# Optimization experiments

Hardware: AMD Instinct MI355X
Metric: run time of the kernel (lower is better)

Reference implementation:

```python
import jax, jax.numpy as jnp
import numpy as np

NEG_SLOPE = 0.2  # PyG GATConv default LeakyReLU slope


def _leaky_relu(x):
    return jnp.where(x >= 0, x, NEG_SLOPE * x)


def gat_conv(x, edge_index, W, a_src, a_dst, b, concat):
    """Faithful PyG GATConv: gather -> leakyrelu attention -> per-dst softmax -> scatter.
    x: [N, Fin], edge_index: [2, E] (src, dst), W: [Fin, H*C], a_src/a_dst: [H, C], b: [H*C] or [C].
    """
    N = x.shape[0]
    H, C = a_src.shape
    src, dst = edge_index[0], edge_index[1]
    h = (x @ W).reshape(N, H, C)                       # [N, H, C]
    alpha_s = jnp.einsum('nhc,hc->nh', h, a_src)       # [N, H]
    alpha_d = jnp.einsum('nhc,hc->nh', h, a_dst)       # [N, H]
    e = _leaky_relu(alpha_s[src] + alpha_d[dst])       # [E, H]
    # numerically stable softmax over edges grouped by destination node
    m = jax.ops.segment_max(e, dst, num_segments=N)    # [N, H]
    e = jnp.exp(e - m[dst])                            # [E, H]
    denom = jax.ops.segment_sum(e, dst, num_segments=N)  # [N, H]
    alpha = e / denom[dst]                             # [E, H]
    msg = h[src] * alpha[:, :, None]                   # [E, H, C]
    out = jax.ops.segment_sum(msg, dst, num_segments=N)  # [N, H, C]
    out = out.reshape(N, H * C) if concat else out.mean(axis=1)
    return out + b


def setup_inputs() -> dict:
    key = jax.random.key(0)
    ks = jax.random.split(key, 12)
    N, E, Fin, Fout = 100000, 1600000, 256, 40
    H1, C1 = 8, 8
    x = jax.random.normal(ks[0], (N, Fin), dtype=jnp.float32)
    edge_index = jax.random.randint(ks[1], (2, E), 0, N, dtype=jnp.int64)
    g = lambda k, shape: jax.random.normal(k, shape, dtype=jnp.float32) * np.float32(np.sqrt(2.0 / (shape[0] + shape[-1])))
    return {
        'x': x,
        'edge_index': edge_index,
        'W1': g(ks[2], (Fin, H1 * C1)),
        'a1_src': g(ks[3], (H1, C1)),
        'a1_dst': g(ks[4], (H1, C1)),
        'b1': jnp.zeros((H1 * C1,), dtype=jnp.float32),
        'W2': g(ks[5], (H1 * C1, Fout)),
        'a2_src': g(ks[6], (1, Fout)),
        'a2_dst': g(ks[7], (1, Fout)),
        'b2': jnp.zeros((Fout,), dtype=jnp.float32),
    }


def reference(x, edge_index, W1, a1_src, a1_dst, b1, W2, a2_src, a2_dst, b2):
    N = x.shape[0]
    # PyG GATConv adds self-loops by default
    loops = jnp.arange(N, dtype=edge_index.dtype)
    ei = jnp.concatenate([edge_index, jnp.stack([loops, loops])], axis=1)
    h = gat_conv(x, ei, W1, a1_src, a1_dst, b1, concat=True)   # [N, 64]
    h = jax.nn.relu(h)  # F.dropout is identity in eval mode
    h = gat_conv(h, ei, W2, a2_src, a2_dst, b2, concat=False)  # [N, Fout]
    return jax.nn.log_softmax(h, axis=1)
```

## Files before the change

### kernel.cpp

```cpp
#include <hip/hip_runtime.h>
#include <math.h>

#define NEG_SLOPE 0.2f
__device__ __forceinline__ float lrelu(float x){ return x >= 0.f ? x : NEG_SLOPE * x; }

typedef __attribute__((ext_vector_type(8))) short bf16x8;
typedef __attribute__((ext_vector_type(4))) float f32x4;

__device__ __forceinline__ float wred_sum(float v){
  #pragma unroll
  for (int o = 32; o; o >>= 1) v += __shfl_xor(v, o, 64);
  return v;
}

__device__ __forceinline__ float bfhi_f(float f){
  return __uint_as_float(__float_as_uint(f) & 0xFFFF0000u);
}
__device__ __forceinline__ unsigned short f2bf(float f){
  unsigned u = __float_as_uint(f);
  unsigned r = u + 0x7FFFu + ((u >> 16) & 1u);
  return (unsigned short)(r >> 16);
}

__global__ __launch_bounds__(256) void k_prep(const int* __restrict__ ei, int E, int N, int nb, int cb,
    unsigned* __restrict__ bcnt,
    const float* __restrict__ W1, short* __restrict__ wt_hi, short* __restrict__ wt_lo,
    const float* __restrict__ W2, short* __restrict__ wt2_hi, short* __restrict__ wt2_lo){
  __shared__ unsigned h[512];
  int bid = blockIdx.x;
  if (bid < cb){
    const int tot = E + N;
    for (int i = threadIdx.x; i < nb; i += 256) h[i] = 0;
    __syncthreads();
    int base = bid * 8192;
    #pragma unroll 4
    for (int j = 0; j < 32; j++){
      int e = base + threadIdx.x + j * 256;
      if (e < tot){
        unsigned d = (e < E) ? (unsigned)ei[E + e] : (unsigned)(e - E);
        atomicAdd(&h[d >> 8], 1u);
      }
    }
    __syncthreads();
    for (int i = threadIdx.x; i < nb; i += 256)
      if (h[i]) atomicAdd(&bcnt[i], h[i]);
  } else if (bid < cb + 64){
    int i = (bid - cb) * 256 + threadIdx.x;
    int k = i >> 6, c = i & 63;
    float v = W1[i];
    unsigned u = __float_as_uint(v);
    wt_hi[c * 256 + k] = (short)(u >> 16);
    float lo = v - bfhi_f(v);
    wt_lo[c * 256 + k] = (short)(__float_as_uint(lo) >> 16);
  } else {
    int i = (bid - cb - 64) * 256 + threadIdx.x;
    if (i < 48 * 64){
      int c = i >> 6, k = i & 63;
      float v = (c < 40) ? W2[k * 40 + c] : 0.f;
      unsigned u = __float_as_uint(v);
      wt2_hi[c * 64 + k] = (short)(u >> 16);
      float l = v - bfhi_f(v);
      wt2_lo[c * 64 + k] = (short)(__float_as_uint(l) >> 16);
    }
  }
}

__global__ void k_bscan(const unsigned* __restrict__ bcnt, unsigned* __restrict__ bbase,
                        unsigned* __restrict__ bcur, int nb, int tot){
  __shared__ unsigned s[512];
  int t = threadIdx.x;
  unsigned v = (t < nb) ? bcnt[t] : 0u;
  s[t] = v; __syncthreads();
  for (int off = 1; off < 512; off <<= 1){
    unsigned x = (t >= off) ? s[t - off] : 0u; __syncthreads();
    s[t] += x; __syncthreads();
  }
  if (t < nb){ unsigned b = s[t] - v; bbase[t] = b; bcur[t] = b; }
  if (t == 0) bbase[nb] = (unsigned)tot;
}

__global__ __launch_bounds__(256) void k_binscat(const int* __restrict__ ei, int E, int N, int nb,
    unsigned* __restrict__ bcur, unsigned* __restrict__ staged){
  __shared__ unsigned sd[8192];
  __shared__ unsigned hist[512];
  __shared__ unsigned runb[512];
  const int tot = E + N;
  for (int i = threadIdx.x; i < nb; i += 256) hist[i] = 0;
  __syncthreads();
  int base = blockIdx.x * 8192;
  #pragma unroll 4
  for (int j = 0; j < 32; j++){
    int idx = threadIdx.x + j * 256;
    int e = base + idx;
    unsigned d = 0xFFFFFFFFu;
    if (e < tot) d = (e < E) ? (unsigned)ei[E + e] : (unsigned)(e - E);
    sd[idx] = d;
    if (d != 0xFFFFFFFFu) atomicAdd(&hist[d >> 8], 1u);
  }
  __syncthreads();
  for (int i = threadIdx.x; i < nb; i += 256){
    unsigned c = hist[i];
    runb[i] = c ? atomicAdd(&bcur[i], c) : 0u;
    hist[i] = 0;
  }
  __syncthreads();
  #pragma unroll 4
  for (int j = 0; j < 32; j++){
    int idx = threadIdx.x + j * 256;
    unsigned d = sd[idx];
    if (d == 0xFFFFFFFFu) continue;
    int e = base + idx;
    unsigned s = (e < E) ? (unsigned)ei[e] : d;
    unsigned b = d >> 8;
    unsigned pos = runb[b] + atomicAdd(&hist[b], 1u);
    staged[pos] = s | ((d & 255u) << 20);
  }
}

__global__ __launch_bounds__(256) void k_csrgemm1(
    const unsigned* __restrict__ bbase, const unsigned* __restrict__ staged, int nb,
    unsigned* __restrict__ off_, unsigned* __restrict__ cur, int* __restrict__ srcids,
    const float* __restrict__ x,
    const unsigned* __restrict__ wtu_hi, const unsigned* __restrict__ wtu_lo,
    const float* __restrict__ a1s, const float* __restrict__ a1d,
    unsigned short* __restrict__ h1b, float* __restrict__ as_, float* __restrict__ ad_, int N){
  __shared__ union {
    struct { unsigned cnt[256], scn[256], cnt2[256]; } c;
    unsigned B[2][64 * 132];
  } sm;

  if (blockIdx.x < nb){
    int b = blockIdx.x, t = threadIdx.x;
    unsigned beg = bbase[b], end = bbase[b + 1];
    sm.c.cnt[t] = 0; sm.c.cnt2[t] = 0;
    __syncthreads();
    for (unsigned i = beg + t; i < end; i += 256)
      atomicAdd(&sm.c.cnt[staged[i] >> 20], 1u);
    __syncthreads();
    unsigned v = sm.c.cnt[t];
    sm.c.scn[t] = v; __syncthreads();
    for (int off = 1; off < 256; off <<= 1){
      unsigned xval = (t >= off) ? sm.c.scn[t - off] : 0u; __syncthreads();
      sm.c.scn[t] += xval; __syncthreads();
    }
    unsigned ex = sm.c.scn[t] - v;
    int d = b * 256 + t;
    if (d < N){ off_[d] = beg + ex; cur[d] = beg + ex + v; }
    sm.c.cnt[t] = ex;
    __syncthreads();
    for (unsigned i = beg + t; i < end; i += 256){
      unsigned u = staged[i];
      unsigned dl = u >> 20;
      unsigned pos = beg + sm.c.cnt[dl] + atomicAdd(&sm.c.cnt2[dl], 1u);
      srcids[pos] = (int)(u & 0xFFFFFu);
    }
    return;
  }

  int bid  = blockIdx.x - nb;
  int lane = threadIdx.x & 63;
  int wv   = threadIdx.x >> 6;
  int r0   = bid * 64 + wv * 16;
  int col16 = lane & 15;
  int kg    = lane >> 4;

  #pragma unroll
  for (int j = 0; j < 32; j++){
    int g = threadIdx.x + j * 256;
    int row = g >> 7, col = g & 127;
    sm.B[0][row * 132 + col] = wtu_hi[g];
    sm.B[1][row * 132 + col] = wtu_lo[g];
  }
  __syncthreads();
  if (r0 >= N) return;

  const float* xr = x + (size_t)min(r0 + col16, N - 1) * 256 + kg * 8;

  f32x4 acc[4];
  #pragma unroll
  for (int ct = 0; ct < 4; ct++) acc[ct] = (f32x4){0.f, 0.f, 0.f, 0.f};

  #pragma unroll 2
  for (int kt = 0; kt < 8; kt++){
    float4 v0 = *(const float4*)(xr + kt * 32);
    float4 v1 = *(const float4*)(xr + kt * 32 + 4);
    unsigned u[8] = {__float_as_uint(v0.x), __float_as_uint(v0.y), __float_as_uint(v0.z), __float_as_uint(v0.w),
                     __float_as_uint(v1.x), __float_as_uint(v1.y), __float_as_uint(v1.z), __float_as_uint(v1.w)};
    union { bf16x8 v; unsigned u[4]; } ahi, alo;
    #pragma unroll
    for (int j = 0; j < 4; j++)
      ahi.u[j] = __builtin_amdgcn_perm(u[2*j+1], u[2*j], 0x07060302);
    float lo[8];
    lo[0] = v0.x - bfhi_f(v0.x); lo[1] = v0.y - bfhi_f(v0.y);
    lo[2] = v0.z - bfhi_f(v0.z); lo[3] = v0.w - bfhi_f(v0.w);
    lo[4] = v1.x - bfhi_f(v1.x); lo[5] = v1.y - bfhi_f(v1.y);
    lo[6] = v1.z - bfhi_f(v1.z); lo[7] = v1.w - bfhi_f(v1.w);
    #pragma unroll
    for (int j = 0; j < 4; j++)
      alo.u[j] = __builtin_amdgcn_perm(__float_as_uint(lo[2*j+1]), __float_as_uint(lo[2*j]), 0x07060302);

    #pragma unroll
    for (int ct = 0; ct < 4; ct++){
      int wcol = ct * 16 + col16;
      const bf16x8 bhi = *(const bf16x8*)(&sm.B[0][wcol * 132 + kt * 16 + kg * 4]);
      const bf16x8 blo = *(const bf16x8*)(&sm.B[1][wcol * 132 + kt * 16 + kg * 4]);
      acc[ct] = __builtin_amdgcn_mfma_f32_16x16x32_bf16(ahi.v, bhi, acc[ct], 0, 0, 0);
      acc[ct] = __builtin_amdgcn_mfma_f32_16x16x32_bf16(ahi.v, blo, acc[ct], 0, 0, 0);
      acc[ct] = __builtin_amdgcn_mfma_f32_16x16x32_bf16(alo.v, bhi, acc[ct], 0, 0, 0);
    }
  }

  float cs[4], cd[4];
  #pragma unroll
  for (int ct = 0; ct < 4; ct++){ cs[ct] = a1s[ct * 16 + col16]; cd[ct] = a1d[ct * 16 + col16]; }
  #pragma unroll
  for (int r = 0; r < 4; r++){
    int rr = r0 + kg * 4 + r;
    bool ok = rr < N;
    #pragma unroll
    for (int ct = 0; ct < 4; ct++){
      float v = acc[ct][r];
      if (ok) h1b[(size_t)rr * 64 + ct * 16 + col16] = f2bf(v);
      float s = v * cs[ct];
      float t = v * cd[ct];
      s += __shfl_xor(s, 1, 64); s += __shfl_xor(s, 2, 64); s += __shfl_xor(s, 4, 64);
      t += __shfl_xor(t, 1, 64); t += __shfl_xor(t, 2, 64); t += __shfl_xor(t, 4, 64);
      if (ok && (col16 & 7) == 0){
        int head = ct * 2 + (col16 >> 3);
        as_[(size_t)rr * 8 + head] = s;
        ad_[(size_t)rr * 8 + head] = t;
      }
    }
  }
}

__global__ __launch_bounds__(256) void k_gat1(const unsigned* __restrict__ off_, const unsigned* __restrict__ cur,
    const int* __restrict__ srcids, const float* __restrict__ as_, const float* __restrict__ ad_,
    const unsigned short* __restrict__ h1b, const float* __restrict__ b1,
    unsigned short* __restrict__ out1b, int N){
  int lane = threadIdx.x & 63;
  int wv   = threadIdx.x >> 6;
  int d    = blockIdx.x * 4 + wv;
  if (d >= N) return;
  __shared__ float lds_p[4][64 * 8];
  __shared__ int   lds_s[4][64];
  float* lp = lds_p[wv];
  int*   ls = lds_s[wv];
  unsigned beg = off_[d], fin = cur[d];

  int e8 = lane >> 3, h = lane & 7;
  int c0 = lane & 31, pe = lane >> 5, hh = c0 >> 2;
  float adh = ad_[(size_t)d * 8 + h];
  float psacc = 0.f, accx = 0.f, accy = 0.f;

  for (unsigned base = beg; base < fin; base += 64){
    int nthis = (int)min(64u, fin - base);
    unsigned i = base + lane;
    ls[lane] = (i < fin) ? srcids[i] : 0;
    asm volatile("s_waitcnt lgkmcnt(0)" ::: "memory");
    __builtin_amdgcn_sched_barrier(0);
    for (int j = 0; j < nthis; j += 8){
      int eloc = j + e8;
      int s = ls[eloc];
      float p = 0.f;
      if (eloc < nthis) p = __expf(lrelu(as_[(size_t)s * 8 + h] + adh));
      lp[eloc * 8 + h] = p;
      psacc += p;
    }
    asm volatile("s_waitcnt lgkmcnt(0)" ::: "memory");
    __builtin_amdgcn_sched_barrier(0);
    for (int e = 0; e < nthis; e += 8){
      int e0 = e + pe, e1 = e + 2 + pe, e2 = e + 4 + pe, e3 = e + 6 + pe;
      float p0 = lp[e0 * 8 + hh], p1 = lp[e1 * 8 + hh];
      float p2 = lp[e2 * 8 + hh], p3 = lp[e3 * 8 + hh];
      int s0 = ls[e0], s1 = ls[e1], s2 = ls[e2], s3 = ls[e3];
      unsigned u0 = *(const unsigned*)(h1b + (size_t)s0 * 64 + c0 * 2);
      unsigned u1 = *(const unsigned*)(h1b + (size_t)s1 * 64 + c0 * 2);
      unsigned u2 = *(const unsigned*)(h1b + (size_t)s2 * 64 + c0 * 2);
      unsigned u3 = *(const unsigned*)(h1b + (size_t)s3 * 64 + c0 * 2);
      accx = fmaf(p0, __uint_as_float(u0 << 16), accx);
      accy = fmaf(p0, __uint_as_float(u0 & 0xFFFF0000u), accy);
      accx = fmaf(p1, __uint_as_float(u1 << 16), accx);
      accy = fmaf(p1, __uint_as_float(u1 & 0xFFFF0000u), accy);
      accx = fmaf(p2, __uint_as_float(u2 << 16), accx);
      accy = fmaf(p2, __uint_as_float(u2 & 0xFFFF0000u), accy);
      accx = fmaf(p3, __uint_as_float(u3 << 16), accx);
      accy = fmaf(p3, __uint_as_float(u3 & 0xFFFF0000u), accy);
    }
    asm volatile("" ::: "memory");
  }
  float den = psacc;
  den += __shfl_xor(den, 8, 64);
  den += __shfl_xor(den, 16, 64);
  den += __shfl_xor(den, 32, 64);
  float mydenv = __shfl(den, hh, 64);
  accx += __shfl_xor(accx, 32, 64);
  accy += __shfl_xor(accy, 32, 64);
  if (lane < 32){
    int ch = lane * 2;
    float v0 = accx / mydenv + b1[ch];
    float v1 = accy / mydenv + b1[ch + 1];
    ushort2 o;
    o.x = f2bf(v0 > 0.f ? v0 : 0.f);
    o.y = f2bf(v1 > 0.f ? v1 : 0.f);
    *(ushort2*)(out1b + (size_t)d * 64 + ch) = o;
  }
}

__global__ __launch_bounds__(256) void k_gemm2m(const unsigned short* __restrict__ out1b,
    const short* __restrict__ wt2_hi, const short* __restrict__ wt2_lo,
    const float* __restrict__ a2s, const float* __restrict__ a2d,
    unsigned short* __restrict__ h2b, float* __restrict__ as_, float* __restrict__ ad_, int N){
  int lane = threadIdx.x & 63;
  int wv   = threadIdx.x >> 6;
  int r0   = blockIdx.x * 64 + wv * 16;
  if (r0 >= N) return;
  int col16 = lane & 15;
  int kg    = lane >> 4;
  const unsigned short* ar = out1b + (size_t)min(r0 + col16, N - 1) * 64 + kg * 8;

  f32x4 acc[3];
  #pragma unroll
  for (int ct = 0; ct < 3; ct++) acc[ct] = (f32x4){0.f, 0.f, 0.f, 0.f};

  #pragma unroll
  for (int kt = 0; kt < 2; kt++){
    const bf16x8 a = *(const bf16x8*)(ar + kt * 32);
    #pragma unroll
    for (int ct = 0; ct < 3; ct++){
      int wcol = ct * 16 + col16;
      const bf16x8 bhi = *(const bf16x8*)(wt2_hi + wcol * 64 + kt * 32 + kg * 8);
      const bf16x8 blo = *(const bf16x8*)(wt2_lo + wcol * 64 + kt * 32 + kg * 8);
      acc[ct] = __builtin_amdgcn_mfma_f32_16x16x32_bf16(a, bhi, acc[ct], 0, 0, 0);
      acc[ct] = __builtin_amdgcn_mfma_f32_16x16x32_bf16(a, blo, acc[ct], 0, 0, 0);
    }
  }

  float cs[3], cd[3];
  #pragma unroll
  for (int ct = 0; ct < 3; ct++){
    int col = ct * 16 + col16;
    bool okc = col < 40;
    cs[ct] = okc ? a2s[col] : 0.f;
    cd[ct] = okc ? a2d[col] : 0.f;
  }
  #pragma unroll
  for (int r = 0; r < 4; r++){
    int rr = r0 + kg * 4 + r;
    bool ok = rr < N;
    float s = 0.f, t = 0.f;
    #pragma unroll
    for (int ct = 0; ct < 3; ct++){
      s = fmaf(acc[ct][r], cs[ct], s);
      t = fmaf(acc[ct][r], cd[ct], t);
      int col = ct * 16 + col16;
      if (ok && col < 40) h2b[(size_t)rr * 40 + col] = f2bf(acc[ct][r]);
    }
    s += __shfl_xor(s, 1, 64); s += __shfl_xor(s, 2, 64);
    s += __shfl_xor(s, 4, 64); s += __shfl_xor(s, 8, 64);
    t += __shfl_xor(t, 1, 64); t += __shfl_xor(t, 2, 64);
    t += __shfl_xor(t, 4, 64); t += __shfl_xor(t, 8, 64);
    if (ok && col16 == 0){ as_[rr] = s; ad_[rr] = t; }
  }
}

__global__ __launch_bounds__(256) void k_gat2(const unsigned* __restrict__ off_, const unsigned* __restrict__ cur,
    const int* __restrict__ srcids, const float* __restrict__ as_, const float* __restrict__ ad_,
    const unsigned short* __restrict__ h2b, const float* __restrict__ b2, float* __restrict__ out, int N){
  int lane = threadIdx.x & 63;
  int wv   = threadIdx.x >> 6;
  int d    = blockIdx.x * 4 + wv;
  if (d >= N) return;
  __shared__ float lds_p[4][64];
  __shared__ int   lds_s[4][64];
  float* lp = lds_p[wv];
  int*   ls = lds_s[wv];
  unsigned beg = off_[d], fin = cur[d];
  float add = ad_[d];

  int c0 = lane & 31;
  int pe = lane >> 5;
  int idx = c0 < 20 ? c0 : 19;
  float ps = 0.f, accx = 0.f, accy = 0.f;

  for (unsigned base = beg; base < fin; base += 64){
    unsigned i = base + lane;
    int nthis = (int)min(64u, fin - base);
    if (i < fin){
      int s = srcids[i];
      float p = __expf(lrelu(as_[s] + add));
      ps += p; ls[lane] = s; lp[lane] = p;
    } else { ls[lane] = 0; lp[lane] = 0.f; }
    asm volatile("s_waitcnt lgkmcnt(0)" ::: "memory");
    __builtin_amdgcn_sched_barrier(0);
    for (int e = 0; e < nthis; e += 8){
      int e0 = e + pe, e1 = e + 2 + pe, e2 = e + 4 + pe, e3 = e + 6 + pe;
      float p0 = lp[e0], p1 = lp[e1], p2 = lp[e2], p3 = lp[e3];
      int s0 = ls[e0], s1 = ls[e1], s2 = ls[e2], s3 = ls[e3];
      unsigned u0 = *(const unsigned*)(h2b + (size_t)s0 * 40 + idx * 2);
      unsigned u1 = *(const unsigned*)(h2b + (size_t)s1 * 40 + idx * 2);
      unsigned u2 = *(const unsigned*)(h2b + (size_t)s2 * 40 + idx * 2);
      unsigned u3 = *(const unsigned*)(h2b + (size_t)s3 * 40 + idx * 2);
      accx = fmaf(p0, __uint_as_float(u0 << 16), accx);
      accy = fmaf(p0, __uint_as_float(u0 & 0xFFFF0000u), accy);
      accx = fmaf(p1, __uint_as_float(u1 << 16), accx);
      accy = fmaf(p1, __uint_as_float(u1 & 0xFFFF0000u), accy);
      accx = fmaf(p2, __uint_as_float(u2 << 16), accx);
      accy = fmaf(p2, __uint_as_float(u2 & 0xFFFF0000u), accy);
      accx = fmaf(p3, __uint_as_float(u3 << 16), accx);
      accy = fmaf(p3, __uint_as_float(u3 & 0xFFFF0000u), accy);
    }
    asm volatile("" ::: "memory");
  }
  ps = wred_sum(ps);
  accx += __shfl_xor(accx, 32, 64);
  accy += __shfl_xor(accy, 32, 64);

  float v0 = accx / ps + b2[idx * 2];
  float v1 = accy / ps + b2[idx * 2 + 1];
  bool act = (c0 < 20);
  float mx = act ? fmaxf(v0, v1) : -INFINITY;
  #pragma unroll
  for (int o = 16; o; o >>= 1) mx = fmaxf(mx, __shfl_xor(mx, o, 64));
  float exs = act ? (__expf(v0 - mx) + __expf(v1 - mx)) : 0.f;
  #pragma unroll
  for (int o = 16; o; o >>= 1) exs += __shfl_xor(exs, o, 64);
  float lse = mx + logf(exs);
  if (lane < 20){
    float2 o2; o2.x = v0 - lse; o2.y = v1 - lse;
    *(float2*)(out + (size_t)d * 40 + lane * 2) = o2;
  }
}

extern "C" void kernel_launch(void* const* d_in, const int* in_sizes, int n_in,
                              void* d_out, int out_size, void* d_ws, size_t ws_size,
                              hipStream_t stream){
  const float* x   = (const float*)d_in[0];
  const int*   ei  = (const int*)d_in[1];
  const float* W1  = (const float*)d_in[2];
  const float* a1s = (const float*)d_in[3];
  const float* a1d = (const float*)d_in[4];
  const float* b1  = (const float*)d_in[5];
  const float* W2  = (const float*)d_in[6];
  const float* a2s = (const float*)d_in[7];
  const float* a2d = (const float*)d_in[8];
  const float* b2  = (const float*)d_in[9];
  float* out = (float*)d_out;

  const int N = in_sizes[0] / 256;
  const int E = in_sizes[1] / 2;
  const int tot = E + N;
  const int nb  = (N + 255) >> 8;

  float* ws = (float*)d_ws;
  size_t o = 0;
  float* as1  = ws + o; o += (size_t)N * 8;
  float* ad1  = ws + o; o += (size_t)N * 8;
  unsigned short* out1b = (unsigned short*)(ws + o); o += (size_t)N * 32;
  unsigned short* h1b   = (unsigned short*)(ws + o); o += (size_t)N * 32;
  unsigned short* h2b   = (unsigned short*)(ws + o); o += (size_t)N * 20;
  unsigned* off_ = (unsigned*)(ws + o); o += (size_t)N;
  unsigned* cur  = (unsigned*)(ws + o); o += (size_t)N;
  int* srcids    = (int*)(ws + o);      o += (size_t)tot;
  short* wt_hi   = (short*)(ws + o);    o += 8192;
  short* wt_lo   = (short*)(ws + o);    o += 8192;
  short* wt2_hi  = (short*)(ws + o);    o += 1536;
  short* wt2_lo  = (short*)(ws + o);    o += 1536;
  unsigned* bcnt  = (unsigned*)(ws + o); o += nb;
  unsigned* bbase = (unsigned*)(ws + o); o += nb + 1;
  unsigned* bcur  = (unsigned*)(ws + o); o += nb;
  unsigned* staged = (unsigned*)out1b;
  float* as2 = as1;
  float* ad2 = ad1;

  const int cb = (tot + 8191) / 8192;
  const int gb = (N + 63) / 64;

  hipMemsetAsync(bcnt, 0, sizeof(unsigned) * (size_t)nb, stream);

  k_prep   <<<cb + 64 + 12, 256, 0, stream>>>(ei, E, N, nb, cb, bcnt,
                                              W1, wt_hi, wt_lo, W2, wt2_hi, wt2_lo);
  k_bscan  <<<1, 512, 0, stream>>>(bcnt, bbase, bcur, nb, tot);
  k_binscat<<<cb, 256, 0, stream>>>(ei, E, N, nb, bcur, staged);

  k_csrgemm1<<<nb + gb, 256, 0, stream>>>(bbase, staged, nb, off_, cur, srcids,
                                          x, (const unsigned*)wt_hi, (const unsigned*)wt_lo,
                                          a1s, a1d, h1b, as1, ad1, N);
  k_gat1 <<<(N + 3) / 4, 256, 0, stream>>>(off_, cur, srcids, as1, ad1, h1b, b1, out1b, N);

  k_gemm2m<<<(N + 63) / 64, 256, 0, stream>>>(out1b, wt2_hi, wt2_lo, a2s, a2d, h2b, as2, ad2, N);
  k_gat2  <<<(N + 3) / 4, 256, 0, stream>>>(off_, cur, srcids, as2, ad2, h2b, b2, out, N);
}
```

Measured before the change: 225.0 us.

## Fuse layer-2 projection into GAT1 aggregation and widen gather loads

Removes the separate layer-2 GEMM kernel and the out1b intermediate. Each wavefront now writes its aggregated, ReLU'd 64-wide row to LDS and computes the 40-wide W2 projection plus the layer-2 attention logits with scalar FMAs reading W2 from global memory. Both aggregation kernels switch from 2-channel 32-bit gathers to 4-channel 64-bit gathers, covering 4 edges per iteration instead of 2. The cost is per-row FP32 scalar matmul work in place of MFMA, and W2 reads repeated across rows through the cache.

Measured after the change: 248.6 us. +10.5%, slower.

```diff
diff --git a/kernel.cpp b/kernel.cpp
--- a/kernel.cpp
+++ b/kernel.cpp
@@ -24,8 +24,7 @@
 
 __global__ __launch_bounds__(256) void k_prep(const int* __restrict__ ei, int E, int N, int nb, int cb,
     unsigned* __restrict__ bcnt,
-    const float* __restrict__ W1, short* __restrict__ wt_hi, short* __restrict__ wt_lo,
-    const float* __restrict__ W2, short* __restrict__ wt2_hi, short* __restrict__ wt2_lo){
+    const float* __restrict__ W1, short* __restrict__ wt_hi, short* __restrict__ wt_lo){
   __shared__ unsigned h[512];
   int bid = blockIdx.x;
   if (bid < cb){
@@ -44,7 +43,7 @@
     __syncthreads();
     for (int i = threadIdx.x; i < nb; i += 256)
       if (h[i]) atomicAdd(&bcnt[i], h[i]);
-  } else if (bid < cb + 64){
+  } else {
     int i = (bid - cb) * 256 + threadIdx.x;
     int k = i >> 6, c = i & 63;
     float v = W1[i];
@@ -52,16 +51,6 @@
     wt_hi[c * 256 + k] = (short)(u >> 16);
     float lo = v - bfhi_f(v);
     wt_lo[c * 256 + k] = (short)(__float_as_uint(lo) >> 16);
-  } else {
-    int i = (bid - cb - 64) * 256 + threadIdx.x;
-    if (i < 48 * 64){
-      int c = i >> 6, k = i & 63;
-      float v = (c < 40) ? W2[k * 40 + c] : 0.f;
-      unsigned u = __float_as_uint(v);
-      wt2_hi[c * 64 + k] = (short)(u >> 16);
-      float l = v - bfhi_f(v);
-      wt2_lo[c * 64 + k] = (short)(__float_as_uint(l) >> 16);
-    }
   }
 }
 
@@ -237,29 +226,34 @@
 __global__ __launch_bounds__(256) void k_gat1(const unsigned* __restrict__ off_, const unsigned* __restrict__ cur,
     const int* __restrict__ srcids, const float* __restrict__ as_, const float* __restrict__ ad_,
     const unsigned short* __restrict__ h1b, const float* __restrict__ b1,
-    unsigned short* __restrict__ out1b, int N){
+    const float* __restrict__ W2, const float* __restrict__ a2s, const float* __restrict__ a2d,
+    unsigned short* __restrict__ h2b, float* __restrict__ as2, float* __restrict__ ad2, int N){
   int lane = threadIdx.x & 63;
   int wv   = threadIdx.x >> 6;
   int d    = blockIdx.x * 4 + wv;
   if (d >= N) return;
   __shared__ float lds_p[4][64 * 8];
   __shared__ int   lds_s[4][64];
+  __shared__ float lds_r[4][64];
   float* lp = lds_p[wv];
   int*   ls = lds_s[wv];
+  float* lr = lds_r[wv];
   unsigned beg = off_[d], fin = cur[d];
 
   int e8 = lane >> 3, h = lane & 7;
-  int c0 = lane & 31, pe = lane >> 5, hh = c0 >> 2;
+  int cq = lane & 15, qe = lane >> 4, hh2 = cq >> 1;
   float adh = ad_[(size_t)d * 8 + h];
-  float psacc = 0.f, accx = 0.f, accy = 0.f;
+  float psacc = 0.f;
+  float a0 = 0.f, a1 = 0.f, a2v = 0.f, a3 = 0.f;
 
   for (unsigned base = beg; base < fin; base += 64){
     int nthis = (int)min(64u, fin - base);
+    int nthis16 = (nthis + 15) & ~15;
     unsigned i = base + lane;
     ls[lane] = (i < fin) ? srcids[i] : 0;
     asm volatile("s_waitcnt lgkmcnt(0)" ::: "memory");
     __builtin_amdgcn_sched_barrier(0);
-    for (int j = 0; j < nthis; j += 8){
+    for (int j = 0; j < nthis16; j += 8){
       int eloc = j + e8;
       int s = ls[eloc];
       float p = 0.f;
@@ -269,23 +263,18 @@
     }
     asm volatile("s_waitcnt lgkmcnt(0)" ::: "memory");
     __builtin_amdgcn_sched_barrier(0);
-    for (int e = 0; e < nthis; e += 8){
-      int e0 = e + pe, e1 = e + 2 + pe, e2 = e + 4 + pe, e3 = e + 6 + pe;
-      float p0 = lp[e0 * 8 + hh], p1 = lp[e1 * 8 + hh];
-      float p2 = lp[e2 * 8 + hh], p3 = lp[e3 * 8 + hh];
-      int s0 = ls[e0], s1 = ls[e1], s2 = ls[e2], s3 = ls[e3];
-      unsigned u0 = *(const unsigned*)(h1b + (size_t)s0 * 64 + c0 * 2);
-      unsigned u1 = *(const unsigned*)(h1b + (size_t)s1 * 64 + c0 * 2);
-      unsigned u2 = *(const unsigned*)(h1b + (size_t)s2 * 64 + c0 * 2);
-      unsigned u3 = *(const unsigned*)(h1b + (size_t)s3 * 64 + c0 * 2);
-      accx = fmaf(p0, __uint_as_float(u0 << 16), accx);
-      accy = fmaf(p0, __uint_as_float(u0 & 0xFFFF0000u), accy);
-      accx = fmaf(p1, __uint_as_float(u1 << 16), accx);
-      accy = fmaf(p1, __uint_as_float(u1 & 0xFFFF0000u), accy);
-      accx = fmaf(p2, __uint_as_float(u2 << 16), accx);
-      accy = fmaf(p2, __uint_as_float(u2 & 0xFFFF0000u), accy);
-      accx = fmaf(p3, __uint_as_float(u3 << 16), accx);
-      accy = fmaf(p3, __uint_as_float(u3 & 0xFFFF0000u), accy);
+    for (int e = 0; e < nthis; e += 16){
+      #pragma unroll
+      for (int j = 0; j < 4; j++){
+        int ee = e + j * 4 + qe;
+        float pv = lp[ee * 8 + hh2];
+        int se = ls[ee];
+        uint2 u = *(const uint2*)(h1b + (size_t)se * 64 + cq * 4);
+        a0  = fmaf(pv, __uint_as_float(u.x << 16), a0);
+        a1  = fmaf(pv, __uint_as_float(u.x & 0xFFFF0000u), a1);
+        a2v = fmaf(pv, __uint_as_float(u.y << 16), a2v);
+        a3  = fmaf(pv, __uint_as_float(u.y & 0xFFFF0000u), a3);
+      }
     }
     asm volatile("" ::: "memory");
   }
@@ -293,75 +282,35 @@
   den += __shfl_xor(den, 8, 64);
   den += __shfl_xor(den, 16, 64);
   den += __shfl_xor(den, 32, 64);
-  float mydenv = __shfl(den, hh, 64);
-  accx += __shfl_xor(accx, 32, 64);
-  accy += __shfl_xor(accy, 32, 64);
-  if (lane < 32){
-    int ch = lane * 2;
-    float v0 = accx / mydenv + b1[ch];
-    float v1 = accy / mydenv + b1[ch + 1];
-    ushort2 o;
-    o.x = f2bf(v0 > 0.f ? v0 : 0.f);
-    o.y = f2bf(v1 > 0.f ? v1 : 0.f);
-    *(ushort2*)(out1b + (size_t)d * 64 + ch) = o;
-  }
-}
-
-__global__ __launch_bounds__(256) void k_gemm2m(const unsigned short* __restrict__ out1b,
-    const short* __restrict__ wt2_hi, const short* __restrict__ wt2_lo,
-    const float* __restrict__ a2s, const float* __restrict__ a2d,
-    unsigned short* __restrict__ h2b, float* __restrict__ as_, float* __restrict__ ad_, int N){
-  int lane = threadIdx.x & 63;
-  int wv   = threadIdx.x >> 6;
-  int r0   = blockIdx.x * 64 + wv * 16;
-  if (r0 >= N) return;
-  int col16 = lane & 15;
-  int kg    = lane >> 4;
-  const unsigned short* ar = out1b + (size_t)min(r0 + col16, N - 1) * 64 + kg * 8;
-
-  f32x4 acc[3];
-  #pragma unroll
-  for (int ct = 0; ct < 3; ct++) acc[ct] = (f32x4){0.f, 0.f, 0.f, 0.f};
-
-  #pragma unroll
-  for (int kt = 0; kt < 2; kt++){
-    const bf16x8 a = *(const bf16x8*)(ar + kt * 32);
-    #pragma unroll
-    for (int ct = 0; ct < 3; ct++){
-      int wcol = ct * 16 + col16;
-      const bf16x8 bhi = *(const bf16x8*)(wt2_hi + wcol * 64 + kt * 32 + kg * 8);
-      const bf16x8 blo = *(const bf16x8*)(wt2_lo + wcol * 64 + kt * 32 + kg * 8);
-      acc[ct] = __builtin_amdgcn_mfma_f32_16x16x32_bf16(a, bhi, acc[ct], 0, 0, 0);
-      acc[ct] = __builtin_amdgcn_mfma_f32_16x16x32_bf16(a, blo, acc[ct], 0, 0, 0);
-    }
-  }
-
-  float cs[3], cd[3];
-  #pragma unroll
-  for (int ct = 0; ct < 3; ct++){
-    int col = ct * 16 + col16;
-    bool okc = col < 40;
-    cs[ct] = okc ? a2s[col] : 0.f;
-    cd[ct] = okc ? a2d[col] : 0.f;
-  }
-  #pragma unroll
-  for (int r = 0; r < 4; r++){
-    int rr = r0 + kg * 4 + r;
-    bool ok = rr < N;
-    float s = 0.f, t = 0.f;
-    #pragma unroll
-    for (int ct = 0; ct < 3; ct++){
-      s = fmaf(acc[ct][r], cs[ct], s);
-      t = fmaf(acc[ct][r], cd[ct], t);
-      int col = ct * 16 + col16;
-      if (ok && col < 40) h2b[(size_t)rr * 40 + col] = f2bf(acc[ct][r]);
-    }
-    s += __shfl_xor(s, 1, 64); s += __shfl_xor(s, 2, 64);
-    s += __shfl_xor(s, 4, 64); s += __shfl_xor(s, 8, 64);
-    t += __shfl_xor(t, 1, 64); t += __shfl_xor(t, 2, 64);
-    t += __shfl_xor(t, 4, 64); t += __shfl_xor(t, 8, 64);
-    if (ok && col16 == 0){ as_[rr] = s; ad_[rr] = t; }
-  }
+  float mydenv = __shfl(den, hh2, 64);
+  a0 += __shfl_xor(a0, 16, 64);  a0 += __shfl_xor(a0, 32, 64);
+  a1 += __shfl_xor(a1, 16, 64);  a1 += __shfl_xor(a1, 32, 64);
+  a2v += __shfl_xor(a2v, 16, 64); a2v += __shfl_xor(a2v, 32, 64);
+  a3 += __shfl_xor(a3, 16, 64);  a3 += __shfl_xor(a3, 32, 64);
+
+  if (lane < 16){
+    float4 r;
+    r.x = fmaxf(a0 / mydenv + b1[cq * 4 + 0], 0.f);
+    r.y = fmaxf(a1 / mydenv + b1[cq * 4 + 1], 0.f);
+    r.z = fmaxf(a2v / mydenv + b1[cq * 4 + 2], 0.f);
+    r.w = fmaxf(a3 / mydenv + b1[cq * 4 + 3], 0.f);
+    *(float4*)(lr + cq * 4) = r;
+  }
+  asm volatile("s_waitcnt lgkmcnt(0)" ::: "memory");
+  __builtin_amdgcn_sched_barrier(0);
+
+  int c = lane;
+  int ci = c < 40 ? c : 39;
+  float hv = 0.f;
+  #pragma unroll 8
+  for (int k = 0; k < 64; k++)
+    hv = fmaf(lr[k], W2[k * 40 + ci], hv);
+  if (c >= 40) hv = 0.f;
+  if (c < 40) h2b[(size_t)d * 40 + c] = f2bf(hv);
+  float s2 = hv * a2s[ci];
+  float t2 = hv * a2d[ci];
+  s2 = wred_sum(s2); t2 = wred_sum(t2);
+  if (lane == 0){ as2[d] = s2; ad2[d] = t2; }
 }
 
 __global__ __launch_bounds__(256) void k_gat2(const unsigned* __restrict__ off_, const unsigned* __restrict__ cur,
@@ -378,10 +327,10 @@
   unsigned beg = off_[d], fin = cur[d];
   float add = ad_[d];
 
-  int c0 = lane & 31;
-  int pe = lane >> 5;
-  int idx = c0 < 20 ? c0 : 19;
-  float ps = 0.f, accx = 0.f, accy = 0.f;
+  int cq = lane & 15, qe = lane >> 4;
+  int ci = cq < 10 ? cq : 9;
+  float ps = 0.f;
+  float a0 = 0.f, a1 = 0.f, a2v = 0.f, a3 = 0.f;
 
   for (unsigned base = beg; base < fin; base += 64){
     unsigned i = base + lane;
@@ -393,42 +342,43 @@
     } else { ls[lane] = 0; lp[lane] = 0.f; }
     asm volatile("s_waitcnt lgkmcnt(0)" ::: "memory");
     __builtin_amdgcn_sched_barrier(0);
-    for (int e = 0; e < nthis; e += 8){
-      int e0 = e + pe, e1 = e + 2 + pe, e2 = e + 4 + pe, e3 = e + 6 + pe;
-      float p0 = lp[e0], p1 = lp[e1], p2 = lp[e2], p3 = lp[e3];
-      int s0 = ls[e0], s1 = ls[e1], s2 = ls[e2], s3 = ls[e3];
-      unsigned u0 = *(const unsigned*)(h2b + (size_t)s0 * 40 + idx * 2);
-      unsigned u1 = *(const unsigned*)(h2b + (size_t)s1 * 40 + idx * 2);
-      unsigned u2 = *(const unsigned*)(h2b + (size_t)s2 * 40 + idx * 2);
-      unsigned u3 = *(const unsigned*)(h2b + (size_t)s3 * 40 + idx * 2);
-      accx = fmaf(p0, __uint_as_float(u0 << 16), accx);
-      accy = fmaf(p0, __uint_as_float(u0 & 0xFFFF0000u), accy);
-      accx = fmaf(p1, __uint_as_float(u1 << 16), accx);
-      accy = fmaf(p1, __uint_as_float(u1 & 0xFFFF0000u), accy);
-      accx = fmaf(p2, __uint_as_float(u2 << 16), accx);
-      accy = fmaf(p2, __uint_as_float(u2 & 0xFFFF0000u), accy);
-      accx = fmaf(p3, __uint_as_float(u3 << 16), accx);
-      accy = fmaf(p3, __uint_as_float(u3 & 0xFFFF0000u), accy);
+    for (int e = 0; e < nthis; e += 16){
+      #pragma unroll
+      for (int j = 0; j < 4; j++){
+        int ee = e + j * 4 + qe;
+        float pv = lp[ee];
+        int se = ls[ee];
+        uint2 u = *(const uint2*)(h2b + (size_t)se * 40 + ci * 4);
+        a0  = fmaf(pv, __uint_as_float(u.x << 16), a0);
+        a1  = fmaf(pv, __uint_as_float(u.x & 0xFFFF0000u), a1);
+        a2v = fmaf(pv, __uint_as_float(u.y << 16), a2v);
+        a3  = fmaf(pv, __uint_as_float(u.y & 0xFFFF0000u), a3);
+      }
     }
     asm volatile("" ::: "memory");
   }
   ps = wred_sum(ps);
-  accx += __shfl_xor(accx, 32, 64);
-  accy += __shfl_xor(accy, 32, 64);
-
-  float v0 = accx / ps + b2[idx * 2];
-  float v1 = accy / ps + b2[idx * 2 + 1];
-  bool act = (c0 < 20);
-  float mx = act ? fmaxf(v0, v1) : -INFINITY;
-  #pragma unroll
-  for (int o = 16; o; o >>= 1) mx = fmaxf(mx, __shfl_xor(mx, o, 64));
-  float exs = act ? (__expf(v0 - mx) + __expf(v1 - mx)) : 0.f;
-  #pragma unroll
-  for (int o = 16; o; o >>= 1) exs += __shfl_xor(exs, o, 64);
+  a0 += __shfl_xor(a0, 16, 64);  a0 += __shfl_xor(a0, 32, 64);
+  a1 += __shfl_xor(a1, 16, 64);  a1 += __shfl_xor(a1, 32, 64);
+  a2v += __shfl_xor(a2v, 16, 64); a2v += __shfl_xor(a2v, 32, 64);
+  a3 += __shfl_xor(a3, 16, 64);  a3 += __shfl_xor(a3, 32, 64);
+
+  float v0 = a0 / ps + b2[ci * 4 + 0];
+  float v1 = a1 / ps + b2[ci * 4 + 1];
+  float v2 = a2v / ps + b2[ci * 4 + 2];
+  float v3 = a3 / ps + b2[ci * 4 + 3];
+  bool act = (cq < 10);
+  float mx = act ? fmaxf(fmaxf(v0, v1), fmaxf(v2, v3)) : -INFINITY;
+  #pragma unroll
+  for (int o = 8; o; o >>= 1) mx = fmaxf(mx, __shfl_xor(mx, o, 64));
+  float exs = act ? (__expf(v0 - mx) + __expf(v1 - mx) + __expf(v2 - mx) + __expf(v3 - mx)) : 0.f;
+  #pragma unroll
+  for (int o = 8; o; o >>= 1) exs += __shfl_xor(exs, o, 64);
   float lse = mx + logf(exs);
-  if (lane < 20){
-    float2 o2; o2.x = v0 - lse; o2.y = v1 - lse;
-    *(float2*)(out + (size_t)d * 40 + lane * 2) = o2;
+  if (lane < 16 && cq < 10){
+    float4 o4;
+    o4.x = v0 - lse; o4.y = v1 - lse; o4.z = v2 - lse; o4.w = v3 - lse;
+    *(float4*)(out + (size_t)d * 40 + cq * 4) = o4;
   }
 }
 
@@ -456,38 +406,33 @@
   size_t o = 0;
   float* as1  = ws + o; o += (size_t)N * 8;
   float* ad1  = ws + o; o += (size_t)N * 8;
-  unsigned short* out1b = (unsigned short*)(ws + o); o += (size_t)N * 32;
-  unsigned short* h1b   = (unsigned short*)(ws + o); o += (size_t)N * 32;
-  unsigned short* h2b   = (unsigned short*)(ws + o); o += (size_t)N * 20;
+  unsigned* staged = (unsigned*)(ws + o); o += (size_t)tot;
+  unsigned short* h1b = (unsigned short*)(ws + o); o += (size_t)N * 32;
+  unsigned short* h2b = (unsigned short*)(ws + o); o += (size_t)N * 20;
+  float* as2 = ws + o; o += (size_t)N;
+  float* ad2 = ws + o; o += (size_t)N;
   unsigned* off_ = (unsigned*)(ws + o); o += (size_t)N;
   unsigned* cur  = (unsigned*)(ws + o); o += (size_t)N;
   int* srcids    = (int*)(ws + o);      o += (size_t)tot;
   short* wt_hi   = (short*)(ws + o);    o += 8192;
   short* wt_lo   = (short*)(ws + o);    o += 8192;
-  short* wt2_hi  = (short*)(ws + o);    o += 1536;
-  short* wt2_lo  = (short*)(ws + o);    o += 1536;
   unsigned* bcnt  = (unsigned*)(ws + o); o += nb;
   unsigned* bbase = (unsigned*)(ws + o); o += nb + 1;
   unsigned* bcur  = (unsigned*)(ws + o); o += nb;
-  unsigned* staged = (unsigned*)out1b;
-  float* as2 = as1;
-  float* ad2 = ad1;
 
   const int cb = (tot + 8191) / 8192;
   const int gb = (N + 63) / 64;
 
   hipMemsetAsync(bcnt, 0, sizeof(unsigned) * (size_t)nb, stream);
 
-  k_prep   <<<cb + 64 + 12, 256, 0, stream>>>(ei, E, N, nb, cb, bcnt,
-                                              W1, wt_hi, wt_lo, W2, wt2_hi, wt2_lo);
+  k_prep   <<<cb + 64, 256, 0, stream>>>(ei, E, N, nb, cb, bcnt, W1, wt_hi, wt_lo);
   k_bscan  <<<1, 512, 0, stream>>>(bcnt, bbase, bcur, nb, tot);
   k_binscat<<<cb, 256, 0, stream>>>(ei, E, N, nb, bcur, staged);
 
   k_csrgemm1<<<nb + gb, 256, 0, stream>>>(bbase, staged, nb, off_, cur, srcids,
                                           x, (const unsigned*)wt_hi, (const unsigned*)wt_lo,
                                           a1s, a1d, h1b, as1, ad1, N);
-  k_gat1 <<<(N + 3) / 4, 256, 0, stream>>>(off_, cur, srcids, as1, ad1, h1b, b1, out1b, N);
-
-  k_gemm2m<<<(N + 63) / 64, 256, 0, stream>>>(out1b, wt2_hi, wt2_lo, a2s, a2d, h2b, as2, ad2, N);
-  k_gat2  <<<(N + 3) / 4, 256, 0, stream>>>(off_, cur, srcids, as2, ad2, h2b, b2, out, N);
-}
+  k_gat1 <<<(N + 3) / 4, 256, 0, stream>>>(off_, cur, srcids, as1, ad1, h1b, b1,
+                                           W2, a2s, a2d, h2b, as2, ad2, N);
+  k_gat2 <<<(N + 3) / 4, 256, 0, stream>>>(off_, cur, srcids, as2, ad2, h2b, b2, out, N);
+}
```
